# Kernel optimization log

Measured on AMD Instinct MI355X. Metric: run time of the kernel, lower is better.

The kernel has to match this reference:

```python
import jax, jax.numpy as jnp
import numpy as np

LN_EPS = 1e-5
NORM_EPS = 1e-12
TEMPERATURE = 0.5


def _project(h, W1, b1, W2, b2, g, beta):
    # projection head: Linear -> ReLU -> Linear -> LayerNorm, then L2 normalize
    x = jnp.maximum(h @ W1 + b1, 0.0) @ W2 + b2          # [B, P]
    mu = jnp.mean(x, axis=-1, keepdims=True)
    var = jnp.mean(jnp.square(x - mu), axis=-1, keepdims=True)
    x = (x - mu) * jax.lax.rsqrt(var + LN_EPS) * g + beta
    n = jnp.linalg.norm(x, axis=-1, keepdims=True)
    return x / jnp.maximum(n, NORM_EPS)                   # [B, P]


def setup_inputs() -> dict:
    key = jax.random.key(0)
    ks = jax.random.split(key, 8)
    B, H, P, K, NBUF = 16384, 2048, 256, 64, 2000
    Hh = H // 2
    return {
        "hidden_states": jax.random.normal(ks[0], (B, H), jnp.float32),
        "positive_hidden": jax.random.normal(ks[1], (B, H), jnp.float32),
        "neg_buffer": jax.random.normal(ks[2], (NBUF, P), jnp.float32),
        "W1": jax.random.normal(ks[3], (H, Hh), jnp.float32) * (1.0 / np.sqrt(H)),
        "b1": jnp.zeros((Hh,), jnp.float32),
        "W2": jax.random.normal(ks[4], (Hh, P), jnp.float32) * (1.0 / np.sqrt(Hh)),
        "b2": jnp.zeros((P,), jnp.float32),
        "ln_gamma": jnp.ones((P,), jnp.float32),
        "ln_beta": jnp.zeros((P,), jnp.float32),
        "neg_indices": jax.random.randint(ks[5], (B, K), 0, NBUF, jnp.int32),
    }


def reference(hidden_states, positive_hidden, neg_buffer, W1, b1, W2, b2,
              ln_gamma, ln_beta, neg_indices):
    anchors = _project(hidden_states, W1, b1, W2, b2, ln_gamma, ln_beta)      # [B,P]
    positives = _project(positive_hidden, W1, b1, W2, b2, ln_gamma, ln_beta)  # [B,P]
    # negatives are detached in the original (buffer stores .detach() features)
    negs = jax.lax.stop_gradient(neg_buffer)[neg_indices]                      # [B,K,P]
    pos_sim = jnp.einsum('bp,bp->b', anchors, positives) / TEMPERATURE        # [B]
    neg_sims = jnp.einsum('bkp,bp->bk', negs, anchors) / TEMPERATURE          # [B,K]
    logits = jnp.concatenate([pos_sim[:, None], neg_sims], axis=1)            # [B,1+K]
    # cross-entropy with label 0 for every anchor, averaged over the batch
    loss = -jnp.mean(jax.nn.log_softmax(logits, axis=-1)[:, 0])
    return loss
```

## Files before the change

### kernel.cpp

```cpp
#include <hip/hip_runtime.h>
#include <hip/hip_bf16.h>
#include <cstdint>

#define BATCH   16384
#define HDIM    2048
#define HHDIM   1024
#define PDIM    256
#define KNEG    64
#define NBUF    2000
#define M1      (2 * BATCH)

typedef float  f32x4  __attribute__((ext_vector_type(4)));
typedef __bf16 bf16x8 __attribute__((ext_vector_type(8)));

typedef __attribute__((address_space(3))) unsigned int       lds_u32;
typedef __attribute__((address_space(1))) const unsigned int glb_u32;

__device__ __forceinline__ void gload_lds16(const void* g, void* l) {
  __builtin_amdgcn_global_load_lds((glb_u32*)g, (lds_u32*)l, 16, 0, 0);
}

__device__ __forceinline__ float dot4(f32x4 a, f32x4 b) {
  return a[0]*b[0] + a[1]*b[1] + a[2]*b[2] + a[3]*b[3];
}

#define VMCNT(n) asm volatile("s_waitcnt vmcnt(" #n ")" ::: "memory")

__global__ __launch_bounds__(256)
void cast_bf16_kernel(const float* __restrict__ src, __bf16* __restrict__ dst,
                      long n8) {
  long i = (long)blockIdx.x * blockDim.x + threadIdx.x;
  long stride = (long)gridDim.x * blockDim.x;
  for (; i < n8; i += stride) {
    f32x4 a = ((const f32x4*)src)[2 * i];
    f32x4 b = ((const f32x4*)src)[2 * i + 1];
    bf16x8 w;
    for (int j = 0; j < 4; ++j) { w[j] = (__bf16)a[j]; w[4 + j] = (__bf16)b[j]; }
    ((bf16x8*)dst)[i] = w;
  }
}

__global__ void transpose_cast_kernel(const float* __restrict__ src,
                                      __bf16* __restrict__ dst, int K, int N) {
  __shared__ float tile[32][33];
  int bn = blockIdx.x * 32, bk = blockIdx.y * 32;
  int tx = threadIdx.x, ty = threadIdx.y;
  for (int j = 0; j < 32; j += 8)
    tile[ty + j][tx] = src[(size_t)(bk + ty + j) * N + bn + tx];
  __syncthreads();
  for (int j = 0; j < 32; j += 8)
    dst[(size_t)(bn + ty + j) * K + bk + tx] = (__bf16)tile[tx][ty + j];
}

template <int KD, int NBt, bool RELU_OUT, int GRID>
__global__ __launch_bounds__(512)
void gemm_8ph(const __bf16* __restrict__ A, const __bf16* __restrict__ Bt,
              const float* __restrict__ bias, void* __restrict__ Cv) {
  constexpr int KT   = KD / 64;
  constexpr int HALF = 128 * 64;
  constexpr int STEP = 2 * HALF;
  constexpr int NDIM = NBt * 256;

  __shared__ __bf16 lA[2 * STEP];
  __shared__ __bf16 lB[2 * STEP];

  constexpr int Q = GRID / 8;
  int bid = blockIdx.x;
  int swb = (bid & 7) * Q + (bid >> 3);
  const int mb = swb / NBt, nb = swb % NBt;
  const long mrow0 = (long)mb * 256;
  const int  ncol0 = nb * 256;

  const int tid = threadIdx.x;
  const int wid = tid >> 6, lane = tid & 63;
  const int wr = wid >> 2, wc = wid & 3;
  const int fl = lane & 15, fh = lane >> 4;

  int aoff[4][2], boff[2][2];
  #pragma unroll
  for (int mi = 0; mi < 4; ++mi)
    #pragma unroll
    for (int ks = 0; ks < 2; ++ks) {
      int row = wr * 64 + mi * 16 + fl;
      aoff[mi][ks] = row * 64 + (((ks * 4 + fh) ^ (row & 7)) * 8);
    }
  #pragma unroll
  for (int ni = 0; ni < 2; ++ni)
    #pragma unroll
    for (int ks = 0; ks < 2; ++ks) {
      int row = wc * 32 + ni * 16 + fl;
      boff[ni][ks] = row * 64 + (((ks * 4 + fh) ^ (row & 7)) * 8);
    }

  const int r0 = tid >> 3, sl = tid & 7;
  long aS[2][2], bS[2][2];
  #pragma unroll
  for (int h = 0; h < 2; ++h)
    #pragma unroll
    for (int i = 0; i < 2; ++i) {
      int rr = r0 + i * 64;
      int ss = sl ^ (rr & 7);
      aS[h][i] = (mrow0 + h * 128 + rr) * (long)KD + ss * 8;
      bS[h][i] = ((long)(ncol0 + h * 128 + rr)) * KD + ss * 8;
    }
  const int dstw = wid * 512;

  auto stA = [&](int h, int t) {
    __bf16* base = lA + (t & 1) * STEP + h * HALF + dstw;
    gload_lds16(A + aS[h][0] + (long)t * 64, (void*)(base));
    gload_lds16(A + aS[h][1] + (long)t * 64, (void*)(base + 4096));
  };
  auto stB = [&](int h, int t) {
    __bf16* base = lB + (t & 1) * STEP + h * HALF + dstw;
    gload_lds16(Bt + bS[h][0] + (long)t * 64, (void*)(base));
    gload_lds16(Bt + bS[h][1] + (long)t * 64, (void*)(base + 4096));
  };

  bf16x8 areg[4][2], breg[2][2];
  auto loadA = [&](int mh, int s) {
    const __bf16* base = lA + (s & 1) * STEP + mh * HALF;
    #pragma unroll
    for (int mi = 0; mi < 4; ++mi)
      #pragma unroll
      for (int ks = 0; ks < 2; ++ks)
        areg[mi][ks] = *(const bf16x8*)(base + aoff[mi][ks]);
  };
  auto loadB = [&](int nh, int s) {
    const __bf16* base = lB + (s & 1) * STEP + nh * HALF;
    #pragma unroll
    for (int ni = 0; ni < 2; ++ni)
      #pragma unroll
      for (int ks = 0; ks < 2; ++ks)
        breg[ni][ks] = *(const bf16x8*)(base + boff[ni][ks]);
  };

  f32x4 acc[2][2][4][2] = {};

#define MFMA2(mh, nh, mi, ni)                                                 \
  acc[mh][nh][mi][ni] = __builtin_amdgcn_mfma_f32_16x16x32_bf16(              \
      areg[mi][0], breg[ni][0], acc[mh][nh][mi][ni], 0, 0, 0);                \
  acc[mh][nh][mi][ni] = __builtin_amdgcn_mfma_f32_16x16x32_bf16(              \
      areg[mi][1], breg[ni][1], acc[mh][nh][mi][ni], 0, 0, 0);

#define PHASE_MFMA(mh, nh)                                                    \
  __builtin_amdgcn_s_setprio(1);                                              \
  MFMA2(mh, nh, 0, 0) MFMA2(mh, nh, 0, 1)                                     \
  MFMA2(mh, nh, 1, 0) MFMA2(mh, nh, 1, 1)                                     \
  MFMA2(mh, nh, 2, 0) MFMA2(mh, nh, 2, 1)                                     \
  MFMA2(mh, nh, 3, 0) MFMA2(mh, nh, 3, 1)                                     \
  __builtin_amdgcn_s_setprio(0);

  stA(0, 0); stB(0, 0); stA(1, 0); stB(1, 0);
  stA(0, 1); stB(1, 1); stB(0, 1); stA(1, 1);
  VMCNT(8);
  __builtin_amdgcn_s_barrier();
  __builtin_amdgcn_sched_barrier(0);

  for (int s = 0; s < KT; ++s) {
    loadA(0, s); loadB(0, s);
    if (s >= 1 && s + 1 < KT) stB(0, s + 1);
    __builtin_amdgcn_s_barrier();
    PHASE_MFMA(0, 0);
    __builtin_amdgcn_s_barrier();

    loadB(1, s);
    if (s >= 1 && s + 1 < KT) stA(1, s + 1);
    __builtin_amdgcn_s_barrier();
    PHASE_MFMA(0, 1);
    __builtin_amdgcn_s_barrier();

    loadA(1, s);
    if (s + 2 < KT) stA(0, s + 2);
    __builtin_amdgcn_s_barrier();
    PHASE_MFMA(1, 1);
    __builtin_amdgcn_s_barrier();

    loadB(0, s);
    if (s + 2 < KT) stB(1, s + 2);
    __builtin_amdgcn_s_barrier();
    PHASE_MFMA(1, 0);
    if (s + 2 < KT) { VMCNT(4); } else { VMCNT(0); }
    __builtin_amdgcn_s_barrier();
    __builtin_amdgcn_sched_barrier(0);
  }

#undef PHASE_MFMA
#undef MFMA2

  #pragma unroll
  for (int mh = 0; mh < 2; ++mh)
    #pragma unroll
    for (int nh = 0; nh < 2; ++nh)
      #pragma unroll
      for (int ni = 0; ni < 2; ++ni) {
        int col = ncol0 + nh * 128 + wc * 32 + ni * 16 + fl;
        float bv = bias[col];
        #pragma unroll
        for (int mi = 0; mi < 4; ++mi)
          #pragma unroll
          for (int r = 0; r < 4; ++r) {
            long row = mrow0 + mh * 128 + wr * 64 + mi * 16 + fh * 4 + r;
            float v = acc[mh][nh][mi][ni][r] + bv;
            if constexpr (RELU_OUT) {
              v = fmaxf(v, 0.0f);
              ((__bf16*)Cv)[row * NDIM + col] = (__bf16)v;
            } else {
              ((float*)Cv)[row * NDIM + col] = v;
            }
          }
      }
}

__device__ __forceinline__ int swz(int row) { return (row >> 1) & 3; }

template <int KD, int NB, bool AF32, bool RELU_OUT>
__global__ __launch_bounds__(256)
void gemm_mfma(const void* __restrict__ A0v, const void* __restrict__ A1v,
               const __bf16* __restrict__ Bt, const float* __restrict__ bias,
               void* __restrict__ Cv) {
  __shared__ __bf16 lA[128 * 32];
  __shared__ __bf16 lB[128 * 32];

  const int total_wg = (M1 / 128) * NB;
  int bid = blockIdx.x;
  const int q = total_wg >> 3;
  int swzb = (bid & 7) * q + (bid >> 3);
  const int mb = swzb / NB, nb = swzb % NB;
  const int mrow0 = mb * 128, ncol0 = nb * 128;
  const int NDIM = NB * 128;

  const int tid = threadIdx.x;
  const int wid = tid >> 6, lane = tid & 63;
  const int wr = wid >> 1, wc = wid & 1;
  const int fl = lane & 15, fh = lane >> 4;

  const float*  Af = nullptr;
  const __bf16* Ab = nullptr;
  if constexpr (AF32) {
    const float* A0 = (const float*)A0v;
    const float* A1 = (const float*)A1v;
    Af = (mrow0 < BATCH) ? (A0 + (size_t)mrow0 * KD)
                         : (A1 + (size_t)(mrow0 - BATCH) * KD);
  } else {
    Ab = (const __bf16*)A0v + (size_t)mrow0 * KD;
  }

  f32x4 acc[4][4] = {};
  const int a_row  = wid * 32 + (lane >> 2);
  const int a_slot = lane & 3;

  const int KT = KD / 32;
  for (int kt = 0; kt < KT; ++kt) {
    f32x4 av[2][2];
    if constexpr (AF32) {
      const float* ap = Af + (size_t)a_row * KD + kt * 32 + a_slot * 8;
      av[0][0] = *(const f32x4*)(ap);
      av[0][1] = *(const f32x4*)(ap + 4);
      av[1][0] = *(const f32x4*)(ap + (size_t)16 * KD);
      av[1][1] = *(const f32x4*)(ap + (size_t)16 * KD + 4);
    }
    __syncthreads();
    {
      int chunk = wid * 2;
      for (int c = 0; c < 2; ++c, ++chunk) {
        int row = chunk * 16 + (lane >> 2);
        int sslot = (lane & 3) ^ swz(row);
        const __bf16* srcp = Bt + (size_t)(ncol0 + row) * KD + kt * 32 + sslot * 8;
        gload_lds16(srcp, (void*)(lB + chunk * 512));
      }
    }
    if constexpr (AF32) {
      for (int r = 0; r < 2; ++r) {
        int row = a_row + r * 16;
        int sslot = a_slot ^ swz(row);
        bf16x8 w;
        for (int j = 0; j < 4; ++j) {
          w[j]     = (__bf16)av[r][0][j];
          w[4 + j] = (__bf16)av[r][1][j];
        }
        *(bf16x8*)(lA + row * 32 + sslot * 8) = w;
      }
    } else {
      int chunk = wid * 2;
      for (int c = 0; c < 2; ++c, ++chunk) {
        int row = chunk * 16 + (lane >> 2);
        int sslot = (lane & 3) ^ swz(row);
        const __bf16* srcp = Ab + (size_t)row * KD + kt * 32 + sslot * 8;
        gload_lds16(srcp, (void*)(lA + chunk * 512));
      }
    }
    __syncthreads();

    bf16x8 afr[4], bfr[4];
    for (int mi = 0; mi < 4; ++mi) {
      int row = wr * 64 + mi * 16 + fl;
      afr[mi] = *(const bf16x8*)(lA + row * 32 + (fh ^ swz(row)) * 8);
    }
    for (int ni = 0; ni < 4; ++ni) {
      int row = wc * 64 + ni * 16 + fl;
      bfr[ni] = *(const bf16x8*)(lB + row * 32 + (fh ^ swz(row)) * 8);
    }
    for (int mi = 0; mi < 4; ++mi)
      for (int ni = 0; ni < 4; ++ni)
        acc[mi][ni] = __builtin_amdgcn_mfma_f32_16x16x32_bf16(
            afr[mi], bfr[ni], acc[mi][ni], 0, 0, 0);
  }

  for (int ni = 0; ni < 4; ++ni) {
    int col = ncol0 + wc * 64 + ni * 16 + fl;
    float bv = bias[col];
    for (int mi = 0; mi < 4; ++mi) {
      for (int r = 0; r < 4; ++r) {
        size_t row = (size_t)mrow0 + wr * 64 + mi * 16 + fh * 4 + r;
        float v = acc[mi][ni][r] + bv;
        if constexpr (RELU_OUT) {
          v = fmaxf(v, 0.0f);
          ((__bf16*)Cv)[row * NDIM + col] = (__bf16)v;
        } else {
          ((float*)Cv)[row * NDIM + col] = v;
        }
      }
    }
  }
}

__global__ __launch_bounds__(256)
void ln_l2_kernel(float* __restrict__ X, const float* __restrict__ g,
                  const float* __restrict__ be) {
  int row  = blockIdx.x * 4 + (threadIdx.x >> 6);
  int lane = threadIdx.x & 63;
  float* xp = X + (size_t)row * PDIM + lane * 4;
  f32x4 v = *(const f32x4*)xp;

  float s = v[0] + v[1] + v[2] + v[3];
  for (int m = 1; m < 64; m <<= 1) s += __shfl_xor(s, m, 64);
  float mu = s * (1.0f / PDIM);

  f32x4 d;
  for (int j = 0; j < 4; ++j) d[j] = v[j] - mu;
  float qv = dot4(d, d);
  for (int m = 1; m < 64; m <<= 1) qv += __shfl_xor(qv, m, 64);
  float rs = rsqrtf(qv * (1.0f / PDIM) + 1e-5f);

  f32x4 g4 = *(const f32x4*)(g + lane * 4);
  f32x4 b4 = *(const f32x4*)(be + lane * 4);
  f32x4 y;
  for (int j = 0; j < 4; ++j) y[j] = d[j] * rs * g4[j] + b4[j];

  float n2 = dot4(y, y);
  for (int m = 1; m < 64; m <<= 1) n2 += __shfl_xor(n2, m, 64);
  float sc = 1.0f / fmaxf(sqrtf(n2), 1e-12f);
  for (int j = 0; j < 4; ++j) y[j] *= sc;
  *(f32x4*)xp = y;
}

__global__ __launch_bounds__(256)
void loss_kernel(const float* __restrict__ X, const float* __restrict__ negbuf,
                 const int* __restrict__ nidx, float* __restrict__ partials) {
  __shared__ float lsum[4];
  int b    = blockIdx.x * 4 + (threadIdx.x >> 6);
  int lane = threadIdx.x & 63;
  int g = lane >> 4, lg = lane & 15;

  const float* arow = X + (size_t)b * PDIM;
  const float* prow = X + (size_t)(BATCH + b) * PDIM;

  f32x4 a4[4];
  for (int j = 0; j < 4; ++j) a4[j] = *(const f32x4*)(arow + lg * 16 + j * 4);

  float ps = 0.0f;
  for (int j = 0; j < 4; ++j) {
    f32x4 p = *(const f32x4*)(prow + lg * 16 + j * 4);
    ps += dot4(a4[j], p);
  }
  for (int m = 1; m < 16; m <<= 1) ps += __shfl_xor(ps, m, 64);
  float pos = ps * 2.0f;

  float myneg = -3.0e38f;
  for (int k4 = 0; k4 < 16; ++k4) {
    int k = k4 * 4 + g;
    int idx = nidx[(size_t)b * KNEG + k];
    const float* nrow = negbuf + (size_t)idx * PDIM;
    float sv = 0.0f;
    for (int j = 0; j < 4; ++j) {
      f32x4 nv = *(const f32x4*)(nrow + lg * 16 + j * 4);
      sv += dot4(a4[j], nv);
    }
    for (int m = 1; m < 16; m <<= 1) sv += __shfl_xor(sv, m, 64);
    if (lg == k4) myneg = sv * 2.0f;
  }

  float mx = myneg;
  for (int m = 1; m < 64; m <<= 1) mx = fmaxf(mx, __shfl_xor(mx, m, 64));
  mx = fmaxf(mx, pos);
  float e = expf(myneg - mx);
  for (int m = 1; m < 64; m <<= 1) e += __shfl_xor(e, m, 64);
  float tot = e + expf(pos - mx);
  float lb = -(pos - mx - logf(tot));

  if (lane == 0) lsum[threadIdx.x >> 6] = lb;
  __syncthreads();
  if (threadIdx.x == 0)
    partials[blockIdx.x] = lsum[0] + lsum[1] + lsum[2] + lsum[3];
}

__global__ void finalize_kernel(const float* __restrict__ partials,
                                float* __restrict__ out) {
  __shared__ float ls[4];
  int tid = threadIdx.x;
  float s = 0.0f;
  for (int i = tid; i < 4096; i += 256) s += partials[i];
  for (int m = 1; m < 64; m <<= 1) s += __shfl_xor(s, m, 64);
  if ((tid & 63) == 0) ls[tid >> 6] = s;
  __syncthreads();
  if (tid == 0) out[0] = (ls[0] + ls[1] + ls[2] + ls[3]) * (1.0f / BATCH);
}

extern "C" void kernel_launch(void* const* d_in, const int* in_sizes, int n_in,
                              void* d_out, int out_size, void* d_ws, size_t ws_size,
                              hipStream_t stream) {
  const float* hidden   = (const float*)d_in[0];
  const float* positive = (const float*)d_in[1];
  const float* negbuf   = (const float*)d_in[2];
  const float* W1       = (const float*)d_in[3];
  const float* b1       = (const float*)d_in[4];
  const float* W2       = (const float*)d_in[5];
  const float* b2       = (const float*)d_in[6];
  const float* gamma    = (const float*)d_in[7];
  const float* beta     = (const float*)d_in[8];
  const int*   nidx     = (const int*)d_in[9];
  float* out = (float*)d_out;

  char* ws = (char*)d_ws;

  const size_t OFF_Y1   = 134217728;
  const size_t OFF_W1T  = OFF_Y1 + 67108864;
  const size_t OFF_W2T  = OFF_W1T + 4194304;
  const size_t OFF_PART = OFF_W2T + 524288;
  const size_t NEED_BIG = OFF_PART + 16384;

  const bool big = (ws_size >= NEED_BIG);

  __bf16* W1T; __bf16* W2T; __bf16* Y1; float* X; float* partials;
  __bf16* Abf = nullptr;
  if (big) {
    Abf      = (__bf16*)(ws);
    Y1       = (__bf16*)(ws + OFF_Y1);
    W1T      = (__bf16*)(ws + OFF_W1T);
    W2T      = (__bf16*)(ws + OFF_W2T);
    partials = (float*) (ws + OFF_PART);
    X        = (float*) (ws);
  } else {
    W1T      = (__bf16*)(ws);
    W2T      = (__bf16*)(ws + 4194304);
    Y1       = (__bf16*)(ws + 4718592);
    X        = (float*) (ws + 71827456);
    partials = (float*) (ws + 105381888);
  }

  transpose_cast_kernel<<<dim3(HHDIM / 32, HDIM / 32), dim3(32, 8), 0, stream>>>(
      W1, W1T, HDIM, HHDIM);
  transpose_cast_kernel<<<dim3(PDIM / 32, HHDIM / 32), dim3(32, 8), 0, stream>>>(
      W2, W2T, HHDIM, PDIM);

  if (big) {
    const long n8 = (long)BATCH * HDIM / 8;
    cast_bf16_kernel<<<2048, 256, 0, stream>>>(hidden, Abf, n8);
    cast_bf16_kernel<<<2048, 256, 0, stream>>>(positive, Abf + (size_t)BATCH * HDIM, n8);

    gemm_8ph<HDIM, HHDIM / 256, true, (M1 / 256) * (HHDIM / 256)>
        <<<(M1 / 256) * (HHDIM / 256), 512, 0, stream>>>(Abf, W1T, b1, Y1);

    gemm_8ph<HHDIM, PDIM / 256, false, (M1 / 256) * (PDIM / 256)>
        <<<(M1 / 256) * (PDIM / 256), 512, 0, stream>>>(Y1, W2T, b2, X);
  } else {
    gemm_mfma<HDIM, HHDIM / 128, true, true>
        <<<(M1 / 128) * (HHDIM / 128), 256, 0, stream>>>(
            hidden, positive, W1T, b1, Y1);
    gemm_mfma<HHDIM, PDIM / 128, false, false>
        <<<(M1 / 128) * (PDIM / 128), 256, 0, stream>>>(
            Y1, nullptr, W2T, b2, X);
  }

  ln_l2_kernel<<<M1 / 4, 256, 0, stream>>>(X, gamma, beta);
  loss_kernel<<<BATCH / 4, 256, 0, stream>>>(X, negbuf, nidx, partials);
  finalize_kernel<<<1, 256, 0, stream>>>(partials, out);
}
```

Measured before the change: 348.9 us.

## Double-buffer B fragments, add explicit lgkmcnt waits, halve M tile for second GEMM

The 8-phase GEMM now holds B fragments in two register sets, so the last phase reuses breg0 instead of reloading B from LDS, and explicit lgkmcnt waits plus sched barriers control when LDS reads complete relative to the MFMAs. The kernel gains a BMH template parameter. The second GEMM (N=256) uses a 128-row M tile, which doubles its grid from 128 to 256 blocks and improves CU occupancy. The cost is more registers for the extra B buffer and fragile hand-tuned vmcnt/lgkmcnt counts.

```diff
diff --git a/kernel.cpp b/kernel.cpp
--- a/kernel.cpp
+++ b/kernel.cpp
@@ -25,6 +25,7 @@
 }
 
 #define VMCNT(n) asm volatile("s_waitcnt vmcnt(" #n ")" ::: "memory")
+#define LGKM(n)  asm volatile("s_waitcnt lgkmcnt(" #n ")" ::: "memory")
 
 __global__ __launch_bounds__(256)
 void cast_bf16_kernel(const float* __restrict__ src, __bf16* __restrict__ dst,
@@ -52,23 +53,27 @@
     dst[(size_t)(bn + ty + j) * K + bk + tx] = (__bf16)tile[tx][ty + j];
 }
 
-template <int KD, int NBt, bool RELU_OUT, int GRID>
+template <int KD, int BMH, int NBt, bool RELU_OUT, int GRID>
 __global__ __launch_bounds__(512)
 void gemm_8ph(const __bf16* __restrict__ A, const __bf16* __restrict__ Bt,
               const float* __restrict__ bias, void* __restrict__ Cv) {
-  constexpr int KT   = KD / 64;
-  constexpr int HALF = 128 * 64;
-  constexpr int STEP = 2 * HALF;
-  constexpr int NDIM = NBt * 256;
-
-  __shared__ __bf16 lA[2 * STEP];
-  __shared__ __bf16 lB[2 * STEP];
+  constexpr int KT    = KD / 64;
+  constexpr int MI    = BMH / 32;
+  constexpr int AHALF = BMH * 64;
+  constexpr int BHALF = 128 * 64;
+  constexpr int ASTEP = 2 * AHALF;
+  constexpr int BSTEP = 2 * BHALF;
+  constexpr int NDIM  = NBt * 256;
+  constexpr int AUL   = BMH / 64;
+
+  __shared__ __bf16 lA[2 * ASTEP];
+  __shared__ __bf16 lB[2 * BSTEP];
 
   constexpr int Q = GRID / 8;
   int bid = blockIdx.x;
   int swb = (bid & 7) * Q + (bid >> 3);
   const int mb = swb / NBt, nb = swb % NBt;
-  const long mrow0 = (long)mb * 256;
+  const long mrow0 = (long)mb * (2 * BMH);
   const int  ncol0 = nb * 256;
 
   const int tid = threadIdx.x;
@@ -76,12 +81,12 @@
   const int wr = wid >> 2, wc = wid & 3;
   const int fl = lane & 15, fh = lane >> 4;
 
-  int aoff[4][2], boff[2][2];
+  int aoff[MI][2], boff[2][2];
   #pragma unroll
-  for (int mi = 0; mi < 4; ++mi)
+  for (int mi = 0; mi < MI; ++mi)
     #pragma unroll
     for (int ks = 0; ks < 2; ++ks) {
-      int row = wr * 64 + mi * 16 + fl;
+      int row = wr * (BMH / 2) + mi * 16 + fl;
       aoff[mi][ks] = row * 64 + (((ks * 4 + fh) ^ (row & 7)) * 8);
     }
   #pragma unroll
@@ -93,99 +98,118 @@
     }
 
   const int r0 = tid >> 3, sl = tid & 7;
-  long aS[2][2], bS[2][2];
+  long aS[2][AUL], bS[2][2];
   #pragma unroll
-  for (int h = 0; h < 2; ++h)
+  for (int h = 0; h < 2; ++h) {
+    #pragma unroll
+    for (int i = 0; i < AUL; ++i) {
+      int rr = r0 + i * 64;
+      int ss = sl ^ (rr & 7);
+      aS[h][i] = (mrow0 + h * BMH + rr) * (long)KD + ss * 8;
+    }
     #pragma unroll
     for (int i = 0; i < 2; ++i) {
       int rr = r0 + i * 64;
       int ss = sl ^ (rr & 7);
-      aS[h][i] = (mrow0 + h * 128 + rr) * (long)KD + ss * 8;
       bS[h][i] = ((long)(ncol0 + h * 128 + rr)) * KD + ss * 8;
     }
+  }
   const int dstw = wid * 512;
 
   auto stA = [&](int h, int t) {
-    __bf16* base = lA + (t & 1) * STEP + h * HALF + dstw;
-    gload_lds16(A + aS[h][0] + (long)t * 64, (void*)(base));
-    gload_lds16(A + aS[h][1] + (long)t * 64, (void*)(base + 4096));
+    __bf16* base = lA + (t & 1) * ASTEP + h * AHALF + dstw;
+    #pragma unroll
+    for (int i = 0; i < AUL; ++i)
+      gload_lds16(A + aS[h][i] + (long)t * 64, (void*)(base + i * 4096));
   };
   auto stB = [&](int h, int t) {
-    __bf16* base = lB + (t & 1) * STEP + h * HALF + dstw;
-    gload_lds16(Bt + bS[h][0] + (long)t * 64, (void*)(base));
-    gload_lds16(Bt + bS[h][1] + (long)t * 64, (void*)(base + 4096));
+    __bf16* base = lB + (t & 1) * BSTEP + h * BHALF + dstw;
+    #pragma unroll
+    for (int i = 0; i < 2; ++i)
+      gload_lds16(Bt + bS[h][i] + (long)t * 64, (void*)(base + i * 4096));
   };
 
-  bf16x8 areg[4][2], breg[2][2];
+  bf16x8 areg[MI][2], breg0[2][2], breg1[2][2];
   auto loadA = [&](int mh, int s) {
-    const __bf16* base = lA + (s & 1) * STEP + mh * HALF;
-    #pragma unroll
-    for (int mi = 0; mi < 4; ++mi)
+    const __bf16* base = lA + (s & 1) * ASTEP + mh * AHALF;
+    #pragma unroll
+    for (int mi = 0; mi < MI; ++mi)
       #pragma unroll
       for (int ks = 0; ks < 2; ++ks)
         areg[mi][ks] = *(const bf16x8*)(base + aoff[mi][ks]);
   };
-  auto loadB = [&](int nh, int s) {
-    const __bf16* base = lB + (s & 1) * STEP + nh * HALF;
+  auto loadB = [&](bf16x8 (&br)[2][2], int nh, int s) {
+    const __bf16* base = lB + (s & 1) * BSTEP + nh * BHALF;
     #pragma unroll
     for (int ni = 0; ni < 2; ++ni)
       #pragma unroll
       for (int ks = 0; ks < 2; ++ks)
-        breg[ni][ks] = *(const bf16x8*)(base + boff[ni][ks]);
+        br[ni][ks] = *(const bf16x8*)(base + boff[ni][ks]);
   };
 
-  f32x4 acc[2][2][4][2] = {};
-
-#define MFMA2(mh, nh, mi, ni)                                                 \
-  acc[mh][nh][mi][ni] = __builtin_amdgcn_mfma_f32_16x16x32_bf16(              \
-      areg[mi][0], breg[ni][0], acc[mh][nh][mi][ni], 0, 0, 0);                \
-  acc[mh][nh][mi][ni] = __builtin_amdgcn_mfma_f32_16x16x32_bf16(              \
-      areg[mi][1], breg[ni][1], acc[mh][nh][mi][ni], 0, 0, 0);
-
-#define PHASE_MFMA(mh, nh)                                                    \
+  f32x4 acc[2][2][MI][2] = {};
+
+#define PHASE_MFMA(mh, nh, BR)                                                \
   __builtin_amdgcn_s_setprio(1);                                              \
-  MFMA2(mh, nh, 0, 0) MFMA2(mh, nh, 0, 1)                                     \
-  MFMA2(mh, nh, 1, 0) MFMA2(mh, nh, 1, 1)                                     \
-  MFMA2(mh, nh, 2, 0) MFMA2(mh, nh, 2, 1)                                     \
-  MFMA2(mh, nh, 3, 0) MFMA2(mh, nh, 3, 1)                                     \
+  _Pragma("unroll")                                                           \
+  for (int ks = 0; ks < 2; ++ks) {                                            \
+    _Pragma("unroll")                                                         \
+    for (int mi = 0; mi < MI; ++mi) {                                         \
+      _Pragma("unroll")                                                       \
+      for (int ni = 0; ni < 2; ++ni)                                          \
+        acc[mh][nh][mi][ni] = __builtin_amdgcn_mfma_f32_16x16x32_bf16(        \
+            areg[mi][ks], BR[ni][ks], acc[mh][nh][mi][ni], 0, 0, 0);          \
+    }                                                                         \
+  }                                                                           \
   __builtin_amdgcn_s_setprio(0);
 
   stA(0, 0); stB(0, 0); stA(1, 0); stB(1, 0);
   stA(0, 1); stB(1, 1); stB(0, 1); stA(1, 1);
-  VMCNT(8);
+  if constexpr (BMH == 128) { VMCNT(8); } else { VMCNT(6); }
   __builtin_amdgcn_s_barrier();
   __builtin_amdgcn_sched_barrier(0);
 
   for (int s = 0; s < KT; ++s) {
-    loadA(0, s); loadB(0, s);
+    loadA(0, s);
+    loadB(breg0, 0, s);
     if (s >= 1 && s + 1 < KT) stB(0, s + 1);
-    __builtin_amdgcn_s_barrier();
-    PHASE_MFMA(0, 0);
-    __builtin_amdgcn_s_barrier();
-
-    loadB(1, s);
+    if constexpr (BMH == 128) LGKM(8);
+    __builtin_amdgcn_s_barrier();
+    LGKM(0);
+    __builtin_amdgcn_sched_barrier(0);
+    PHASE_MFMA(0, 0, breg0);
+    __builtin_amdgcn_s_barrier();
+
+    loadB(breg1, 1, s);
     if (s >= 1 && s + 1 < KT) stA(1, s + 1);
     __builtin_amdgcn_s_barrier();
-    PHASE_MFMA(0, 1);
+    LGKM(0);
+    __builtin_amdgcn_sched_barrier(0);
+    PHASE_MFMA(0, 1, breg1);
     __builtin_amdgcn_s_barrier();
 
     loadA(1, s);
     if (s + 2 < KT) stA(0, s + 2);
     __builtin_amdgcn_s_barrier();
-    PHASE_MFMA(1, 1);
-    __builtin_amdgcn_s_barrier();
-
-    loadB(0, s);
+    LGKM(0);
+    __builtin_amdgcn_sched_barrier(0);
+    PHASE_MFMA(1, 1, breg1);
+    __builtin_amdgcn_s_barrier();
+
     if (s + 2 < KT) stB(1, s + 2);
     __builtin_amdgcn_s_barrier();
-    PHASE_MFMA(1, 0);
-    if (s + 2 < KT) { VMCNT(4); } else { VMCNT(0); }
-    __builtin_amdgcn_s_barrier();
     __builtin_amdgcn_sched_barrier(0);
+    PHASE_MFMA(1, 0, breg0);
+    if (s + 2 < KT) {
+      if constexpr (BMH == 128) { VMCNT(4); } else { VMCNT(3); }
+    } else {
+      VMCNT(0);
+    }
+    __builtin_amdgcn_s_barrier();
+    __builtin_amdgcn_sched_barrier(0);
   }
 
 #undef PHASE_MFMA
-#undef MFMA2
 
   #pragma unroll
   for (int mh = 0; mh < 2; ++mh)
@@ -196,10 +220,10 @@
         int col = ncol0 + nh * 128 + wc * 32 + ni * 16 + fl;
         float bv = bias[col];
         #pragma unroll
-        for (int mi = 0; mi < 4; ++mi)
+        for (int mi = 0; mi < MI; ++mi)
           #pragma unroll
           for (int r = 0; r < 4; ++r) {
-            long row = mrow0 + mh * 128 + wr * 64 + mi * 16 + fh * 4 + r;
+            long row = mrow0 + mh * BMH + wr * (BMH / 2) + mi * 16 + fh * 4 + r;
             float v = acc[mh][nh][mi][ni][r] + bv;
             if constexpr (RELU_OUT) {
               v = fmaxf(v, 0.0f);
@@ -468,11 +492,11 @@
     cast_bf16_kernel<<<2048, 256, 0, stream>>>(hidden, Abf, n8);
     cast_bf16_kernel<<<2048, 256, 0, stream>>>(positive, Abf + (size_t)BATCH * HDIM, n8);
 
-    gemm_8ph<HDIM, HHDIM / 256, true, (M1 / 256) * (HHDIM / 256)>
+    gemm_8ph<HDIM, 128, HHDIM / 256, true, (M1 / 256) * (HHDIM / 256)>
         <<<(M1 / 256) * (HHDIM / 256), 512, 0, stream>>>(Abf, W1T, b1, Y1);
 
-    gemm_8ph<HHDIM, PDIM / 256, false, (M1 / 256) * (PDIM / 256)>
-        <<<(M1 / 256) * (PDIM / 256), 512, 0, stream>>>(Y1, W2T, b2, X);
+    gemm_8ph<HHDIM, 64, PDIM / 256, false, (M1 / 128) * (PDIM / 256)>
+        <<<(M1 / 128) * (PDIM / 256), 512, 0, stream>>>(Y1, W2T, b2, X);
   } else {
     gemm_mfma<HDIM, HHDIM / 128, true, true>
         <<<(M1 / 128) * (HHDIM / 128), 256, 0, stream>>>(
```

Measured after the change: 339.4 us. 1.03x faster.
